# Optimization experiments

Measured on AMD Instinct MI355X. Metric: run time of the kernel, lower is better.

The kernel has to match this reference:

```python
import jax, jax.numpy as jnp
import numpy as np

H = 512      # hidden_size
HH = H // 2  # per-direction LSTM hidden
C = 4096     # num_classes
T = 32       # num_steps
B = 64
FH, FW = 8, 32


def setup_inputs() -> dict:
    key = jax.random.key(0)
    ks = jax.random.split(key, 12)
    s = 0.02
    return {
        "origin_fmap": jax.random.normal(ks[0], (B, H, FH, FW), dtype=jnp.float32),
        "text": jax.random.randint(ks[1], (B, T), 0, C, dtype=jnp.int32),
        "is_train": 1,
        # embedding: Linear(num_classes -> hidden_size)
        "W_emb": jax.random.normal(ks[2], (H, C), dtype=jnp.float32) * s,
        "b_emb": jax.random.normal(ks[3], (H,), dtype=jnp.float32) * s,
        # LSTM: 2 layers x 2 directions, index = layer*2 + direction (torch layout)
        # gate order i, f, g, o; W_ih: [4, 4*HH, H] (layer-1 input is 2*HH == H)
        "W_ih": jax.random.normal(ks[4], (4, 4 * HH, H), dtype=jnp.float32) * s,
        "W_hh": jax.random.normal(ks[5], (4, 4 * HH, HH), dtype=jnp.float32) * s,
        "b_ih": jax.random.normal(ks[6], (4, 4 * HH), dtype=jnp.float32) * s,
        "b_hh": jax.random.normal(ks[7], (4, 4 * HH), dtype=jnp.float32) * s,
        # generator: Linear(hidden_size -> num_classes)
        "W_gen": jax.random.normal(ks[8], (C, H), dtype=jnp.float32) * s,
        "b_gen": jax.random.normal(ks[9], (C,), dtype=jnp.float32) * s,
    }


def _lstm_cell(x, h, c, Wih, Whh, b):
    # torch LSTM cell: gates = x W_ih^T + h W_hh^T + b_ih + b_hh, order i,f,g,o
    z = x @ Wih.T + h @ Whh.T + b
    i, f, g, o = jnp.split(z, 4, axis=-1)
    c_new = jax.nn.sigmoid(f) * c + jax.nn.sigmoid(i) * jnp.tanh(g)
    h_new = jax.nn.sigmoid(o) * jnp.tanh(c_new)
    return h_new, c_new


def reference(origin_fmap, text, is_train, W_emb, b_emb, W_ih, W_hh, b_ih, b_hh, W_gen, b_gen):
    # Training-mode (teacher-forced) branch of HybridBranch.forward
    bsz = text.shape[0]
    # [B, H, h, w] -> [B, h*w, H]
    fmap = jnp.transpose(origin_fmap, (0, 2, 3, 1)).reshape(bsz, -1, H)
    b = b_ih + b_hh  # [4, 4*HH]
    h0 = jnp.zeros((4, bsz, HH), dtype=fmap.dtype)
    c0 = jnp.zeros((4, bsz, HH), dtype=fmap.dtype)

    def step(carry, tok):
        h, c = carry
        x_t = jax.nn.one_hot(tok, C, dtype=fmap.dtype)          # scatter one-hot
        xe = x_t @ W_emb.T + b_emb                               # [B, H]
        # layer 0, forward / backward directions (seq_len == 1)
        hf, cf = _lstm_cell(xe, h[0], c[0], W_ih[0], W_hh[0], b[0])
        hb, cb = _lstm_cell(xe, h[1], c[1], W_ih[1], W_hh[1], b[1])
        out0 = jnp.concatenate([hf, hb], axis=-1)                # [B, H]
        # layer 1
        hf1, cf1 = _lstm_cell(out0, h[2], c[2], W_ih[2], W_hh[2], b[2])
        hb1, cb1 = _lstm_cell(out0, h[3], c[3], W_ih[3], W_hh[3], b[3])
        out = jnp.concatenate([hf1, hb1], axis=-1)               # [B, H]
        # attention exactly as in source: softmax over dim=1 of [B, 1, L]
        scores = jnp.einsum('bh,blh->bl', out, fmap)[:, None, :]  # [B, 1, L]
        a = jax.nn.softmax(scores, axis=1)                        # singleton dim -> ones (faithful)
        ctx = jnp.einsum('bql,blh->bqh', a, fmap)[:, 0]           # [B, H]
        new_h = jnp.stack([hf, hb, hf1, hb1])
        new_c = jnp.stack([cf, cb, cf1, cb1])
        return (new_h, new_c), ctx

    (_, _), hiddens = jax.lax.scan(step, (h0, c0), text.T)  # hiddens: [T, B, H]
    hiddens = jnp.transpose(hiddens, (1, 0, 2))             # [B, T, H]
    g = hiddens @ W_gen.T + b_gen                           # [B, T, C]
    return g
```

## Files before the change

### kernel.cpp

```cpp
#include <hip/hip_runtime.h>
#include <hip/hip_bf16.h>


constexpr int Hd = 512;
constexpr int Cd = 4096;
constexpr int Bd = 64;
constexpr int Td = 32;
constexpr int Ld = 256;

__global__ __launch_bounds__(256) void reduce_rows(const float* __restrict__ in,
                                                   float* __restrict__ ctx) {
    const int gtid = blockIdx.x * 256 + threadIdx.x;
    const int row  = gtid >> 6;
    const int lane = threadIdx.x & 63;
    const float4 v = reinterpret_cast<const float4*>(in + (size_t)row * Ld)[lane];
    float s = v.x + v.y + v.z + v.w;
    #pragma unroll
    for (int m = 1; m < 64; m <<= 1) s += __shfl_xor(s, m, 64);
    if (lane == 0) ctx[row] = s;
}

template<int CTRL>
__device__ __forceinline__ float ror_add(float v) {
    int r = __builtin_amdgcn_update_dpp(0, __float_as_int(v), CTRL, 0xF, 0xF, false);
    return v + __int_as_float(r);
}

__global__ __launch_bounds__(256, 2) void gemm_bcast(const float* __restrict__ ctx,
                                                     const float* __restrict__ Wgen,
                                                     const float* __restrict__ bgen,
                                                     float* __restrict__ out) {
    __shared__ float part[4 * 64 * 4];
    const int tid   = threadIdx.x;
    const int w     = tid >> 6;
    const int lane  = tid & 63;
    const int cpart = lane >> 4;
    const int hp    = lane & 15;
    const int cblk  = blockIdx.x * 64;
    const int b0    = blockIdx.y * 4;

    const float4* W4 = reinterpret_cast<const float4*>(Wgen);
    const float4* X4 = reinterpret_cast<const float4*>(ctx);

    float4 xr[4][2];
    #pragma unroll
    for (int bb = 0; bb < 4; ++bb)
        #pragma unroll
        for (int j = 0; j < 2; ++j)
            xr[bb][j] = X4[(size_t)(b0 + bb) * 128 + w * 32 + j * 16 + hp];

    #pragma unroll 4
    for (int q = 0; q < 16; ++q) {
        const int c = cblk + q * 4 + cpart;
        const size_t base = (size_t)c * 128 + w * 32 + hp;
        const float4 w0 = W4[base];
        const float4 w1 = W4[base + 16];
        float acc[4];
        #pragma unroll
        for (int bb = 0; bb < 4; ++bb) {
            float a = w0.x * xr[bb][0].x + w0.y * xr[bb][0].y
                    + w0.z * xr[bb][0].z + w0.w * xr[bb][0].w
                    + w1.x * xr[bb][1].x + w1.y * xr[bb][1].y
                    + w1.z * xr[bb][1].z + w1.w * xr[bb][1].w;
            a = ror_add<0x128>(a);
            a = ror_add<0x124>(a);
            a = ror_add<0x122>(a);
            a = ror_add<0x121>(a);
            acc[bb] = a;
        }
        if (hp == 0) {
            reinterpret_cast<float4*>(part)[w * 64 + (q * 4 + cpart)] =
                make_float4(acc[0], acc[1], acc[2], acc[3]);
        }
    }
    __syncthreads();

    const int cl = tid & 63;
    const int bl = tid >> 6;
    float v = part[(0 * 64 + cl) * 4 + bl] + part[(1 * 64 + cl) * 4 + bl]
            + part[(2 * 64 + cl) * 4 + bl] + part[(3 * 64 + cl) * 4 + bl]
            + bgen[cblk + cl];

    float* o = out + (size_t)(b0 + bl) * Td * Cd + cblk + cl;
    #pragma unroll
    for (int t = 0; t < Td; ++t) o[(size_t)t * Cd] = v;
}

extern "C" void kernel_launch(void* const* d_in, const int* in_sizes, int n_in,
                              void* d_out, int out_size, void* d_ws, size_t ws_size,
                              hipStream_t stream) {
    const float* fmap = (const float*)d_in[0];
    const float* Wgen = (const float*)d_in[9];
    const float* bgen = (const float*)d_in[10];
    float* out = (float*)d_out;
    float* ctx = (float*)d_ws;

    reduce_rows<<<dim3((Bd * Hd) / 4), dim3(256), 0, stream>>>(fmap, ctx);
    gemm_bcast<<<dim3(Cd / 64, Bd / 4), dim3(256), 0, stream>>>(ctx, Wgen, bgen, out);
}
```

Before: 27.25 us.

## Fuse row reduction and generator GEMM into one cooperative persistent kernel

Replaces the two launches (fmap row-sum and broadcast GEMM) with a single cooperative kernel of 512 blocks. Each block reduces 64 rows, all blocks meet at a grid-wide barrier, and each block then loops over two GEMM tiles. The aim is to remove one kernel launch and the gap between the two kernels, at the cost of a grid-sync and fewer blocks available to hide the memory latency of the large output write.

```diff
diff --git a/kernel.cpp b/kernel.cpp
--- a/kernel.cpp
+++ b/kernel.cpp
@@ -1,5 +1,8 @@
 #include <hip/hip_runtime.h>
 #include <hip/hip_bf16.h>
+#include <hip/hip_cooperative_groups.h>
+
+namespace cg = cooperative_groups;
 
 
 constexpr int Hd = 512;
@@ -8,17 +11,7 @@
 constexpr int Td = 32;
 constexpr int Ld = 256;
 
-__global__ __launch_bounds__(256) void reduce_rows(const float* __restrict__ in,
-                                                   float* __restrict__ ctx) {
-    const int gtid = blockIdx.x * 256 + threadIdx.x;
-    const int row  = gtid >> 6;
-    const int lane = threadIdx.x & 63;
-    const float4 v = reinterpret_cast<const float4*>(in + (size_t)row * Ld)[lane];
-    float s = v.x + v.y + v.z + v.w;
-    #pragma unroll
-    for (int m = 1; m < 64; m <<= 1) s += __shfl_xor(s, m, 64);
-    if (lane == 0) ctx[row] = s;
-}
+constexpr int NBLK = 512;
 
 template<int CTRL>
 __device__ __forceinline__ float ror_add(float v) {
@@ -26,64 +19,87 @@
     return v + __int_as_float(r);
 }
 
-__global__ __launch_bounds__(256, 2) void gemm_bcast(const float* __restrict__ ctx,
-                                                     const float* __restrict__ Wgen,
-                                                     const float* __restrict__ bgen,
-                                                     float* __restrict__ out) {
+__global__ __launch_bounds__(256, 2) void fused(const float* __restrict__ fmap,
+                                                const float* __restrict__ Wgen,
+                                                const float* __restrict__ bgen,
+                                                float* __restrict__ out,
+                                                float* __restrict__ ctx) {
+    const int tid  = threadIdx.x;
+    const int lane = tid & 63;
+    const int w    = tid >> 6;
+    const int bk   = blockIdx.x;
+
+    {
+        const float4* in4 = reinterpret_cast<const float4*>(fmap);
+        const int row0 = (bk * 4 + w) * 16;
+        #pragma unroll 4
+        for (int r = 0; r < 16; ++r) {
+            const int row = row0 + r;
+            const float4 v = in4[(size_t)row * 64 + lane];
+            float s = v.x + v.y + v.z + v.w;
+            #pragma unroll
+            for (int m = 1; m < 64; m <<= 1) s += __shfl_xor(s, m, 64);
+            if (lane == 0) ctx[row] = s;
+        }
+    }
+
+    cg::this_grid().sync();
+
     __shared__ float part[4 * 64 * 4];
-    const int tid   = threadIdx.x;
-    const int w     = tid >> 6;
-    const int lane  = tid & 63;
     const int cpart = lane >> 4;
     const int hp    = lane & 15;
-    const int cblk  = blockIdx.x * 64;
-    const int b0    = blockIdx.y * 4;
-
     const float4* W4 = reinterpret_cast<const float4*>(Wgen);
     const float4* X4 = reinterpret_cast<const float4*>(ctx);
 
-    float4 xr[4][2];
-    #pragma unroll
-    for (int bb = 0; bb < 4; ++bb)
+    for (int tile = bk; tile < 1024; tile += NBLK) {
+        const int cblk = (tile & 63) * 64;
+        const int b0   = (tile >> 6) * 4;
+
+        float4 xr[4][2];
         #pragma unroll
-        for (int j = 0; j < 2; ++j)
-            xr[bb][j] = X4[(size_t)(b0 + bb) * 128 + w * 32 + j * 16 + hp];
+        for (int bb = 0; bb < 4; ++bb)
+            #pragma unroll
+            for (int j = 0; j < 2; ++j)
+                xr[bb][j] = X4[(size_t)(b0 + bb) * 128 + w * 32 + j * 16 + hp];
 
-    #pragma unroll 4
-    for (int q = 0; q < 16; ++q) {
-        const int c = cblk + q * 4 + cpart;
-        const size_t base = (size_t)c * 128 + w * 32 + hp;
-        const float4 w0 = W4[base];
-        const float4 w1 = W4[base + 16];
-        float acc[4];
-        #pragma unroll
-        for (int bb = 0; bb < 4; ++bb) {
-            float a = w0.x * xr[bb][0].x + w0.y * xr[bb][0].y
-                    + w0.z * xr[bb][0].z + w0.w * xr[bb][0].w
-                    + w1.x * xr[bb][1].x + w1.y * xr[bb][1].y
-                    + w1.z * xr[bb][1].z + w1.w * xr[bb][1].w;
-            a = ror_add<0x128>(a);
-            a = ror_add<0x124>(a);
-            a = ror_add<0x122>(a);
-            a = ror_add<0x121>(a);
-            acc[bb] = a;
+        #pragma unroll 4
+        for (int q = 0; q < 16; ++q) {
+            const int c = cblk + q * 4 + cpart;
+            const size_t base = (size_t)c * 128 + w * 32 + hp;
+            const float4 w0 = W4[base];
+            const float4 w1 = W4[base + 16];
+            float acc[4];
+            #pragma unroll
+            for (int bb = 0; bb < 4; ++bb) {
+                float a = w0.x * xr[bb][0].x + w0.y * xr[bb][0].y
+                        + w0.z * xr[bb][0].z + w0.w * xr[bb][0].w
+                        + w1.x * xr[bb][1].x + w1.y * xr[bb][1].y
+                        + w1.z * xr[bb][1].z + w1.w * xr[bb][1].w;
+                a = ror_add<0x128>(a);
+                a = ror_add<0x124>(a);
+                a = ror_add<0x122>(a);
+                a = ror_add<0x121>(a);
+                acc[bb] = a;
+            }
+            if (hp == 0) {
+                reinterpret_cast<float4*>(part)[w * 64 + (q * 4 + cpart)] =
+                    make_float4(acc[0], acc[1], acc[2], acc[3]);
+            }
         }
-        if (hp == 0) {
-            reinterpret_cast<float4*>(part)[w * 64 + (q * 4 + cpart)] =
-                make_float4(acc[0], acc[1], acc[2], acc[3]);
+        __syncthreads();
+
+        {
+            const int cl = lane;
+            const int bl = w;
+            float v = part[(0 * 64 + cl) * 4 + bl] + part[(1 * 64 + cl) * 4 + bl]
+                    + part[(2 * 64 + cl) * 4 + bl] + part[(3 * 64 + cl) * 4 + bl]
+                    + bgen[cblk + cl];
+            float* o = out + (size_t)(b0 + bl) * Td * Cd + cblk + cl;
+            #pragma unroll
+            for (int t = 0; t < Td; ++t) o[(size_t)t * Cd] = v;
         }
+        __syncthreads();
     }
-    __syncthreads();
-
-    const int cl = tid & 63;
-    const int bl = tid >> 6;
-    float v = part[(0 * 64 + cl) * 4 + bl] + part[(1 * 64 + cl) * 4 + bl]
-            + part[(2 * 64 + cl) * 4 + bl] + part[(3 * 64 + cl) * 4 + bl]
-            + bgen[cblk + cl];
-
-    float* o = out + (size_t)(b0 + bl) * Td * Cd + cblk + cl;
-    #pragma unroll
-    for (int t = 0; t < Td; ++t) o[(size_t)t * Cd] = v;
 }
 
 extern "C" void kernel_launch(void* const* d_in, const int* in_sizes, int n_in,
@@ -95,6 +111,7 @@
     float* out = (float*)d_out;
     float* ctx = (float*)d_ws;
 
-    reduce_rows<<<dim3((Bd * Hd) / 4), dim3(256), 0, stream>>>(fmap, ctx);
-    gemm_bcast<<<dim3(Cd / 64, Bd / 4), dim3(256), 0, stream>>>(ctx, Wgen, bgen, out);
+    void* args[] = {(void*)&fmap, (void*)&Wgen, (void*)&bgen, (void*)&out, (void*)&ctx};
+    hipLaunchCooperativeKernel((const void*)fused, dim3(NBLK), dim3(256),
+                               args, 0, stream);
 }
```

Result: slower. 75.56 us (+177.3%).
